# Performance work log

Measured on AMD Instinct MI355X. Metric: run time of the kernel, lower is better.

The kernel has to match this reference:

```python
import jax, jax.numpy as jnp
import numpy as np

EPS = 1e-5

def _conv(x, w, pad):
    # x: [B,C,H,W] NCHW, w: [O,I,kh,kw] OIHW
    return jax.lax.conv_general_dilated(
        x, w, (1, 1), [(pad, pad), (pad, pad)],
        dimension_numbers=('NCHW', 'OIHW', 'NCHW'))

def _bn(x, g, b, m, v):
    # eval-mode batchnorm folded into scale/shift
    s = g * jax.lax.rsqrt(v + EPS)
    return x * s[None, :, None, None] + (b - m * s)[None, :, None, None]

def _cbr(x, w, g, b, m, v):
    # Convolution block from CornerNet: conv3x3(pad=1, no bias) + BN + ReLU
    return jax.nn.relu(_bn(_conv(x, w, 1), g, b, m, v))


def setup_inputs() -> dict:
    key = jax.random.key(0)
    B, Cin, C, H, W = 4, 256, 256, 128, 128
    kdims = {'up': (C, Cin, 3, 3), 'down': (C, Cin, 3, 3),
             'p': (C, C, 3, 3), 'c1': (C, Cin, 1, 1), 'c2': (C, C, 3, 3)}
    inp = {'x': jax.random.normal(key, (B, Cin, H, W), dtype=jnp.float32)}
    for i, n in enumerate(['up', 'down', 'p', 'c1', 'c2']):
        ks = jax.random.split(jax.random.fold_in(key, i + 1), 5)
        inp['w_' + n] = jax.random.normal(ks[0], kdims[n], dtype=jnp.float32) * 0.02
        inp['g_' + n] = 1.0 + 0.1 * jax.random.normal(ks[1], (C,), dtype=jnp.float32)
        inp['b_' + n] = 0.1 * jax.random.normal(ks[2], (C,), dtype=jnp.float32)
        inp['m_' + n] = 0.1 * jax.random.normal(ks[3], (C,), dtype=jnp.float32)
        inp['v_' + n] = 0.5 + jax.random.uniform(ks[4], (C,), dtype=jnp.float32)
    return inp


def reference(x,
              w_up, g_up, b_up, m_up, v_up,
              w_down, g_down, b_down, m_down, v_down,
              w_p, g_p, b_p, m_p, v_p,
              w_c1, g_c1, b_c1, m_c1, v_c1,
              w_c2, g_c2, b_c2, m_c2, v_c2):
    # up branch: conv-bn-relu then LeftPool (reverse cummax over W) then RightPool (cummax over W)
    up = _cbr(x, w_up, g_up, b_up, m_up, v_up)
    up = jax.lax.cummax(up, axis=3, reverse=True)   # LeftPool
    up = jax.lax.cummax(up, axis=3)                 # RightPool
    # down branch: conv-bn-relu then TopPool (reverse cummax over H) then BottomPool (cummax over H)
    down = _cbr(x, w_down, g_down, b_down, m_down, v_down)
    down = jax.lax.cummax(down, axis=2, reverse=True)  # TopPool
    down = jax.lax.cummax(down, axis=2)                # BottomPool
    # merge path: 3x3 conv + BN on pooled sum
    merge = _bn(_conv(up + down, w_p, 1), g_p, b_p, m_p, v_p)
    # shortcut path: 1x1 conv + BN on input
    bn1 = _bn(_conv(x, w_c1, 0), g_c1, b_c1, m_c1, v_c1)
    relu1 = jax.nn.relu(merge + bn1)
    # output Convolution block
    return _cbr(relu1, w_c2, g_c2, b_c2, m_c2, v_c2)
```

## Files before the change

### kernel.cpp

```cpp
#include <hip/hip_runtime.h>

typedef unsigned short u16;
typedef __attribute__((ext_vector_type(8))) short bf16x8;
typedef __attribute__((ext_vector_type(4))) float f32x4;


__device__ __forceinline__ u16 f2bf(float f) {
  unsigned u = __float_as_uint(f);
  unsigned r = u + 0x7fffu + ((u >> 16) & 1u);
  return (u16)(r >> 16);
}

__device__ __forceinline__ void gll16(const char* g, char* l) {
  __builtin_amdgcn_global_load_lds((const __attribute__((address_space(1))) void*)g,
                                   (__attribute__((address_space(3))) void*)l, 16, 0, 0);
}

__global__ void bn_prep_kernel(const float* __restrict__ g, const float* __restrict__ b,
                               const float* __restrict__ m, const float* __restrict__ v,
                               float* __restrict__ st) {
  int c = threadIdx.x;
  float s = g[c] * rsqrtf(v[c] + 1e-5f);
  st[c] = s;
  st[256 + c] = b[c] - m[c] * s;
}

__global__ void bn_fix_kernel(float* __restrict__ st) {
  int c = threadIdx.x;
  st[2 * 512 + 256 + c] += st[3 * 512 + 256 + c];
  st[3 * 512 + c] = st[3 * 512 + c] / st[2 * 512 + c];
}

__global__ void wprep3_kernel(const float* __restrict__ w, u16* __restrict__ dst) {
  int idx = blockIdx.x * 256 + threadIdx.x;
  int blk = idx >> 13, iu = idx & 8191;
  int co = iu >> 5, w32 = iu & 31, slot = w32 >> 3, e = w32 & 7;
  int q = slot ^ ((co >> 1) & 3);
  int kc = blk & 3, t = blk >> 2;
  int dwi = t % 3, t2 = t / 3, d = t2 % 3, half = t2 / 3;
  int s = d * 3 + dwi;
  int ci = half * 128 + kc * 32 + q * 8 + e;
  dst[idx] = f2bf(w[(co * 256 + ci) * 9 + s]);
}

__global__ void wprep1_kernel(const float* __restrict__ w, u16* __restrict__ dst,
                              const float* __restrict__ ratio) {
  int idx = blockIdx.x * 256 + threadIdx.x;
  int blk = idx >> 13, iu = idx & 8191;
  int co = iu >> 5, w32 = iu & 31, slot = w32 >> 3, e = w32 & 7;
  int q = slot ^ ((co >> 1) & 3);
  int kc = blk & 3, half = blk >> 2;
  int ci = half * 128 + kc * 32 + q * 8 + e;
  dst[idx] = f2bf(w[co * 256 + ci] * ratio[co]);
}

__global__ __launch_bounds__(256) void nchw_to_nhwc_kernel(const float* __restrict__ x,
                                                           char* __restrict__ xb) {
  __shared__ __align__(16) u16 tl[128 * 130];
  int bh = blockIdx.x; int b = bh >> 7, h = bh & 127;
  int t = threadIdx.x;
  for (int half = 0; half < 2; ++half) {
    __syncthreads();
    for (int i = 0; i < 64; ++i) {
      int cil = i * 2 + (t >> 7);
      int ci = half * 128 + cil;
      int w = t & 127;
      tl[w * 130 + cil] = f2bf(x[(size_t)((b * 256 + ci) * 128 + h) * 128 + w]);
    }
    __syncthreads();
    char* plane = xb + (size_t)(b * 128 + h) * 65536 + half * 32768;
    for (int i = 0; i < 32; ++i) {
      int w = i * 4 + (t >> 6);
      int c2 = (t & 63) * 2;
      unsigned v = *(const unsigned*)&tl[w * 130 + c2];
      *(unsigned*)(plane + w * 256 + ((c2 * 2) ^ (((w + 1) & 7) << 4))) = v;
    }
  }
}

__device__ __forceinline__ void conv_pipeline(const char* inB1, const char* inB2,
                                              const char* wA1, const char* wA2,
                                              int h, int nsteps, char* lds,
                                              f32x4 (&acc)[4][4]) {
  const int t = threadIdx.x;
  const int wv = t >> 6, lane = t & 63;
  const int lane15 = lane & 15, q = lane >> 4;
  const int coq = wv >> 1, wh = wv & 1;
  char* ldsB = lds;
  char* ldsA0 = lds + 33280;

  int aOff[4];
#pragma unroll
  for (int f = 0; f < 4; ++f) {
    int ra = coq * 64 + f * 16 + lane15;
    aOff[f] = ra * 64 + ((q ^ ((ra >> 1) & 3)) << 4);
  }
  int wpb[4];
#pragma unroll
  for (int f = 0; f < 4; ++f) wpb[f] = wh * 64 + f * 16 + lane15;

  auto stageA = [&](int step, int buf) {
    const char* src = (step < 72) ? (wA1 + (size_t)step * 16384)
                                  : (wA2 + (size_t)(step - 72) * 16384);
    char* dst = ldsA0 + buf * 16384 + wv * 1024;
    const char* g = src + wv * 1024 + lane * 16;
    gll16(g, dst);
    gll16(g + 8192, dst + 8192);
  };
  auto stageB = [&](const char* plane) {
    if (plane) {
      char* dst = ldsB + 256 + wv * 1024;
      const char* g = plane + wv * 1024 + lane * 16;
#pragma unroll
      for (int r = 0; r < 4; ++r) gll16(g + r * 8192, dst + r * 8192);
      int4 z = {0, 0, 0, 0};
      if (t < 16) *(int4*)(ldsB + t * 16) = z;
      else if (t < 32) *(int4*)(ldsB + 33024 + (t - 16) * 16) = z;
    } else {
      int4 z = {0, 0, 0, 0};
#pragma unroll
      for (int r = 0; r < 4; ++r) *(int4*)(ldsB + r * 8192 + t * 16) = z;
      if (t < 32) *(int4*)(ldsB + 32768 + t * 16) = z;
    }
  };

  int cur = 0, i = 0;
  for (int outer = 0; outer < 6; ++outer) {
    const int half = (outer >= 3) ? 1 : 0;
    const int d = outer - half * 3;
    const int hs = h + d - 1;
    const char* plane = (hs >= 0 && hs < 128)
                            ? inB1 + (size_t)hs * 65536 + (size_t)half * 32768
                            : nullptr;
    stageB(plane);
    if (outer == 0) stageA(0, 0);
    __syncthreads();
#pragma unroll
    for (int dwi = 0; dwi < 3; ++dwi) {
#pragma unroll
      for (int kc = 0; kc < 4; ++kc) {
        if (i + 1 < nsteps) stageA(i + 1, cur ^ 1);
        bf16x8 af[4], bf[4];
        const char* lA = ldsA0 + cur * 16384;
#pragma unroll
        for (int f = 0; f < 4; ++f) af[f] = *(const bf16x8*)(lA + aOff[f]);
#pragma unroll
        for (int f = 0; f < 4; ++f) {
          int wp = wpb[f] + dwi;
          bf[f] = *(const bf16x8*)(ldsB + wp * 256 + ((kc * 64 + q * 16) ^ ((wp & 7) << 4)));
        }
#pragma unroll
        for (int fm = 0; fm < 4; ++fm)
#pragma unroll
          for (int fn = 0; fn < 4; ++fn)
            acc[fm][fn] = __builtin_amdgcn_mfma_f32_16x16x32_bf16(af[fm], bf[fn], acc[fm][fn], 0, 0, 0);
        __syncthreads();
        cur ^= 1;
        ++i;
      }
    }
  }
  if (nsteps > 72) {
    for (int half2 = 0; half2 < 2; ++half2) {
      stageB(inB2 + (size_t)h * 65536 + (size_t)half2 * 32768);
      __syncthreads();
#pragma unroll
      for (int kc = 0; kc < 4; ++kc) {
        if (i + 1 < nsteps) stageA(i + 1, cur ^ 1);
        bf16x8 af[4], bf[4];
        const char* lA = ldsA0 + cur * 16384;
#pragma unroll
        for (int f = 0; f < 4; ++f) af[f] = *(const bf16x8*)(lA + aOff[f]);
#pragma unroll
        for (int f = 0; f < 4; ++f) {
          int wp = wpb[f] + 1;
          bf[f] = *(const bf16x8*)(ldsB + wp * 256 + ((kc * 64 + q * 16) ^ ((wp & 7) << 4)));
        }
#pragma unroll
        for (int fm = 0; fm < 4; ++fm)
#pragma unroll
          for (int fn = 0; fn < 4; ++fn)
            acc[fm][fn] = __builtin_amdgcn_mfma_f32_16x16x32_bf16(af[fm], bf[fn], acc[fm][fn], 0, 0, 0);
        __syncthreads();
        cur ^= 1;
        ++i;
      }
    }
  }
}

__device__ __forceinline__ void zero_acc(f32x4 (&acc)[4][4]) {
  f32x4 z = {0.f, 0.f, 0.f, 0.f};
#pragma unroll
  for (int i = 0; i < 4; ++i)
#pragma unroll
    for (int j = 0; j < 4; ++j) acc[i][j] = z;
}

__device__ __forceinline__ void store_pad_relu(f32x4 (&acc)[4][4], const float* __restrict__ st,
                                               int b, int h, char* __restrict__ out) {
  const int t = threadIdx.x, lane = t & 63, wv = t >> 6;
  const int lane15 = lane & 15, q = lane >> 4, coq = wv >> 1, wh = wv & 1;
  char* plane = out + (size_t)(b * 128 + h) * 65536;
#pragma unroll
  for (int fm = 0; fm < 4; ++fm) {
    int co = coq * 64 + fm * 16 + q * 4;
    float ss[4], tt[4];
#pragma unroll
    for (int r = 0; r < 4; ++r) { ss[r] = st[co + r]; tt[r] = st[256 + co + r]; }
#pragma unroll
    for (int fn = 0; fn < 4; ++fn) {
      int w = wh * 64 + fn * 16 + lane15;
      short4 o;
      o.x = (short)f2bf(fmaxf(acc[fm][fn][0] * ss[0] + tt[0], 0.f));
      o.y = (short)f2bf(fmaxf(acc[fm][fn][1] * ss[1] + tt[1], 0.f));
      o.z = (short)f2bf(fmaxf(acc[fm][fn][2] * ss[2] + tt[2], 0.f));
      o.w = (short)f2bf(fmaxf(acc[fm][fn][3] * ss[3] + tt[3], 0.f));
      *(short4*)(plane + (co >> 7) * 32768 + w * 256 + (((co & 127) * 2) ^ (((w + 1) & 7) << 4))) = o;
    }
  }
}

__global__ __launch_bounds__(512, 4) void conv_up_kernel(const char* __restrict__ xb,
                                                         const char* __restrict__ wp,
                                                         const float* __restrict__ st,
                                                         float* __restrict__ rmax) {
  __shared__ __align__(16) char lds[66048];
  int swz = (blockIdx.x & 7) * 64 + (blockIdx.x >> 3);
  int b = swz >> 7, h = swz & 127;
  f32x4 acc[4][4];
  zero_acc(acc);
  conv_pipeline(xb + (size_t)b * 8388608, nullptr, wp, nullptr, h, 72, lds, acc);

  const int t = threadIdx.x, lane = t & 63, wv = t >> 6;
  const int lane15 = lane & 15, q = lane >> 4, coq = wv >> 1, wh = wv & 1;
  float* rlds = (float*)lds;
  __syncthreads();
#pragma unroll
  for (int fm = 0; fm < 4; ++fm) {
    int co = coq * 64 + fm * 16 + q * 4;
#pragma unroll
    for (int r = 0; r < 4; ++r) {
      float ss = st[co + r], tt = st[256 + co + r];
      float v = 0.f;
#pragma unroll
      for (int fn = 0; fn < 4; ++fn) v = fmaxf(v, acc[fm][fn][r] * ss + tt);
      v = fmaxf(v, __shfl_xor(v, 1));
      v = fmaxf(v, __shfl_xor(v, 2));
      v = fmaxf(v, __shfl_xor(v, 4));
      v = fmaxf(v, __shfl_xor(v, 8));
      if (lane15 == 0) rlds[wh * 256 + co + r] = v;
    }
  }
  __syncthreads();
  if (t < 256) rmax[(size_t)(b * 128 + h) * 256 + t] = fmaxf(rlds[t], rlds[256 + t]);
}

__global__ __launch_bounds__(512, 4) void conv_down_kernel(const char* __restrict__ xb,
                                                           const char* __restrict__ wp,
                                                           const float* __restrict__ st,
                                                           char* __restrict__ out) {
  __shared__ __align__(16) char lds[66048];
  int swz = (blockIdx.x & 7) * 64 + (blockIdx.x >> 3);
  int b = swz >> 7, h = swz & 127;
  f32x4 acc[4][4];
  zero_acc(acc);
  conv_pipeline(xb + (size_t)b * 8388608, nullptr, wp, nullptr, h, 72, lds, acc);
  store_pad_relu(acc, st, b, h, out);
}

__global__ __launch_bounds__(256) void colmax_kernel(const char* __restrict__ dp,
                                                     float* __restrict__ cmax) {
  int bw = blockIdx.x; int b = bw >> 7, w = bw & 127;
  int c = threadIdx.x;
  size_t base = (size_t)b * 8388608 + (size_t)(c >> 7) * 32768 + w * 256 +
                (((c & 127) * 2) ^ (((w + 1) & 7) << 4));
  float m = 0.f;
  for (int h = 0; h < 128; ++h) {
    u16 raw = *(const u16*)(dp + base + (size_t)h * 65536);
    m = fmaxf(m, __uint_as_float(((unsigned)raw) << 16));
  }
  cmax[(size_t)(b * 128 + w) * 256 + c] = m;
}

__global__ __launch_bounds__(256) void pooled_kernel(const float* __restrict__ rmax,
                                                     const float* __restrict__ cmax,
                                                     char* __restrict__ dp) {
  int bh = blockIdx.x; int b = bh >> 7, h = bh & 127;
  int c = threadIdx.x;
  float rm = rmax[(size_t)(b * 128 + h) * 256 + c];
  char* plane = dp + (size_t)(b * 128 + h) * 65536 + (c >> 7) * 32768;
  int cb = (c & 127) * 2;
  for (int w = 0; w < 128; ++w) {
    float v = rm + cmax[(size_t)(b * 128 + w) * 256 + c];
    *(u16*)(plane + w * 256 + (cb ^ (((w + 1) & 7) << 4))) = f2bf(v);
  }
}

__global__ __launch_bounds__(512, 4) void conv_merge_kernel(const char* __restrict__ dp,
                                                            const char* __restrict__ xb,
                                                            const char* __restrict__ wp_p,
                                                            const char* __restrict__ wp_c1,
                                                            const float* __restrict__ st,
                                                            char* __restrict__ out) {
  __shared__ __align__(16) char lds[66048];
  int swz = (blockIdx.x & 7) * 64 + (blockIdx.x >> 3);
  int b = swz >> 7, h = swz & 127;
  f32x4 acc[4][4];
  zero_acc(acc);
  conv_pipeline(dp + (size_t)b * 8388608, xb + (size_t)b * 8388608, wp_p, wp_c1, h, 80, lds, acc);
  store_pad_relu(acc, st, b, h, out);
}

__global__ __launch_bounds__(512, 4) void conv_c2_kernel(const char* __restrict__ relu1,
                                                         const char* __restrict__ wp,
                                                         const float* __restrict__ st,
                                                         float* __restrict__ out) {
  __shared__ __align__(16) char lds[66048];
  int swz = (blockIdx.x & 7) * 64 + (blockIdx.x >> 3);
  int b = swz >> 7, h = swz & 127;
  f32x4 acc[4][4];
  zero_acc(acc);
  conv_pipeline(relu1 + (size_t)b * 8388608, nullptr, wp, nullptr, h, 72, lds, acc);

  const int t = threadIdx.x, lane = t & 63, wv = t >> 6;
  const int lane15 = lane & 15, q = lane >> 4, coq = wv >> 1, wh = wv & 1;
  float* tl = (float*)lds;
  for (int g = 0; g < 16; ++g) {
    __syncthreads();
    if (coq == (g >> 2)) {
      int fm = g & 3;
      int co = coq * 64 + fm * 16 + q * 4;
#pragma unroll
      for (int r = 0; r < 4; ++r) {
        float ss = st[co + r], tt = st[256 + co + r];
#pragma unroll
        for (int fn = 0; fn < 4; ++fn) {
          int w = wh * 64 + fn * 16 + lane15;
          tl[(q * 4 + r) * 132 + w] = fmaxf(acc[fm][fn][r] * ss + tt, 0.f);
        }
      }
    }
    __syncthreads();
    int row = t >> 5, wq = (t & 31) * 4;
    float4 vv = *(float4*)&tl[row * 132 + wq];
    *(float4*)(out + (size_t)((b * 256 + g * 16 + row) * 128 + h) * 128 + wq) = vv;
  }
}

extern "C" void kernel_launch(void* const* d_in, const int* in_sizes, int n_in,
                              void* d_out, int out_size, void* d_ws, size_t ws_size,
                              hipStream_t stream) {
  (void)in_sizes; (void)n_in; (void)out_size; (void)ws_size;
  const float* x    = (const float*)d_in[0];
  const float* w_up = (const float*)d_in[1];
  const float* w_dn = (const float*)d_in[6];
  const float* w_p  = (const float*)d_in[11];
  const float* w_c1 = (const float*)d_in[16];
  const float* w_c2 = (const float*)d_in[21];

  char* ws = (char*)d_ws;
  char* xb    = ws;
  char* dp    = ws + 33554432ull;
  char* relu1 = ws + 67108864ull;
  u16* wp_up  = (u16*)(ws + 100663296ull);
  u16* wp_dn  = (u16*)(ws + 101842944ull);
  u16* wp_p   = (u16*)(ws + 103022592ull);
  u16* wp_c2  = (u16*)(ws + 104202240ull);
  u16* wp_c1  = (u16*)(ws + 105381888ull);
  float* st   = (float*)(ws + 105512960ull);
  float* rmax = (float*)(ws + 105523200ull);
  float* cmax = (float*)(ws + 106047488ull);

  bn_prep_kernel<<<1, 256, 0, stream>>>((const float*)d_in[2], (const float*)d_in[3],
                                        (const float*)d_in[4], (const float*)d_in[5], st);
  bn_prep_kernel<<<1, 256, 0, stream>>>((const float*)d_in[7], (const float*)d_in[8],
                                        (const float*)d_in[9], (const float*)d_in[10], st + 512);
  bn_prep_kernel<<<1, 256, 0, stream>>>((const float*)d_in[12], (const float*)d_in[13],
                                        (const float*)d_in[14], (const float*)d_in[15], st + 1024);
  bn_prep_kernel<<<1, 256, 0, stream>>>((const float*)d_in[17], (const float*)d_in[18],
                                        (const float*)d_in[19], (const float*)d_in[20], st + 1536);
  bn_prep_kernel<<<1, 256, 0, stream>>>((const float*)d_in[22], (const float*)d_in[23],
                                        (const float*)d_in[24], (const float*)d_in[25], st + 2048);
  bn_fix_kernel<<<1, 256, 0, stream>>>(st);

  wprep3_kernel<<<2304, 256, 0, stream>>>(w_up, wp_up);
  wprep3_kernel<<<2304, 256, 0, stream>>>(w_dn, wp_dn);
  wprep3_kernel<<<2304, 256, 0, stream>>>(w_p, wp_p);
  wprep3_kernel<<<2304, 256, 0, stream>>>(w_c2, wp_c2);
  wprep1_kernel<<<256, 256, 0, stream>>>(w_c1, wp_c1, st + 1536);

  nchw_to_nhwc_kernel<<<512, 256, 0, stream>>>(x, xb);

  conv_up_kernel<<<512, 512, 0, stream>>>(xb, (const char*)wp_up, st, rmax);
  conv_down_kernel<<<512, 512, 0, stream>>>(xb, (const char*)wp_dn, st + 512, dp);
  colmax_kernel<<<512, 256, 0, stream>>>(dp, cmax);
  pooled_kernel<<<512, 256, 0, stream>>>(rmax, cmax, dp);
  conv_merge_kernel<<<512, 512, 0, stream>>>(dp, xb, (const char*)wp_p, (const char*)wp_c1,
                                             st + 1024, relu1);
  conv_c2_kernel<<<512, 512, 0, stream>>>(relu1, (const char*)wp_c2, st + 2048, (float*)d_out);
}
```

Before: 429.1 us.

## Split conv kernels across output-channel halves with 256-thread blocks

Each conv kernel now runs a 2D grid where blockIdx.y picks one half of the 256 output channels. Blocks shrink to 256 threads and a smaller LDS footprint. The weight prep kernels lay the weights out per half, and the staging code is rewritten for 256 threads. This doubles block count and aims to raise occupancy, at the cost of loading each input row plane twice, once per channel half.

```diff
diff --git a/kernel.cpp b/kernel.cpp
--- a/kernel.cpp
+++ b/kernel.cpp
@@ -33,24 +33,28 @@
 
 __global__ void wprep3_kernel(const float* __restrict__ w, u16* __restrict__ dst) {
   int idx = blockIdx.x * 256 + threadIdx.x;
-  int blk = idx >> 13, iu = idx & 8191;
-  int co = iu >> 5, w32 = iu & 31, slot = w32 >> 3, e = w32 & 7;
-  int q = slot ^ ((co >> 1) & 3);
-  int kc = blk & 3, t = blk >> 2;
-  int dwi = t % 3, t2 = t / 3, d = t2 % 3, half = t2 / 3;
+  int blk = idx >> 12, iu = idx & 4095;
+  int co_l = iu >> 5, w32 = iu & 31, slot = w32 >> 3, e = w32 & 7;
+  int q = slot ^ ((co_l >> 1) & 3);
+  int cohalf = blk / 72, step = blk % 72;
+  int outer = step / 12, rr = step % 12, dwi = rr >> 2, kc = rr & 3;
+  int half = outer / 3, d = outer % 3;
   int s = d * 3 + dwi;
   int ci = half * 128 + kc * 32 + q * 8 + e;
+  int co = cohalf * 128 + co_l;
   dst[idx] = f2bf(w[(co * 256 + ci) * 9 + s]);
 }
 
 __global__ void wprep1_kernel(const float* __restrict__ w, u16* __restrict__ dst,
                               const float* __restrict__ ratio) {
   int idx = blockIdx.x * 256 + threadIdx.x;
-  int blk = idx >> 13, iu = idx & 8191;
-  int co = iu >> 5, w32 = iu & 31, slot = w32 >> 3, e = w32 & 7;
-  int q = slot ^ ((co >> 1) & 3);
-  int kc = blk & 3, half = blk >> 2;
-  int ci = half * 128 + kc * 32 + q * 8 + e;
+  int blk = idx >> 12, iu = idx & 4095;
+  int co_l = iu >> 5, w32 = iu & 31, slot = w32 >> 3, e = w32 & 7;
+  int q = slot ^ ((co_l >> 1) & 3);
+  int cohalf = blk >> 3, j = blk & 7;
+  int half2 = j >> 2, kc = j & 3;
+  int ci = half2 * 128 + kc * 32 + q * 8 + e;
+  int co = cohalf * 128 + co_l;
   dst[idx] = f2bf(w[co * 256 + ci] * ratio[co]);
 }
 
@@ -78,6 +82,29 @@
   }
 }
 
+__device__ __forceinline__ void stage_a(const char* wA1, const char* wA2, int step,
+                                        char* ldsA0, int buf, int t) {
+  const char* src = (step < 72) ? (wA1 + (size_t)step * 8192)
+                                : (wA2 + (size_t)(step - 72) * 8192);
+  char* dst = ldsA0 + buf * 8192 + t * 16;
+  const char* g = src + t * 16;
+  gll16(g, dst);
+  gll16(g + 4096, dst + 4096);
+}
+
+__device__ __forceinline__ void stage_b(const char* plane, char* ldsB, int t) {
+  if (plane) {
+    char* dst = ldsB + 256 + t * 16;
+    const char* g = plane + t * 16;
+#pragma unroll
+    for (int r = 0; r < 8; ++r) gll16(g + r * 4096, dst + r * 4096);
+  } else {
+    int4 z = {0, 0, 0, 0};
+#pragma unroll
+    for (int r = 0; r < 8; ++r) *(int4*)(ldsB + 256 + r * 4096 + t * 16) = z;
+  }
+}
+
 __device__ __forceinline__ void conv_pipeline(const char* inB1, const char* inB2,
                                               const char* wA1, const char* wA2,
                                               int h, int nsteps, char* lds,
@@ -99,30 +126,11 @@
 #pragma unroll
   for (int f = 0; f < 4; ++f) wpb[f] = wh * 64 + f * 16 + lane15;
 
-  auto stageA = [&](int step, int buf) {
-    const char* src = (step < 72) ? (wA1 + (size_t)step * 16384)
-                                  : (wA2 + (size_t)(step - 72) * 16384);
-    char* dst = ldsA0 + buf * 16384 + wv * 1024;
-    const char* g = src + wv * 1024 + lane * 16;
-    gll16(g, dst);
-    gll16(g + 8192, dst + 8192);
-  };
-  auto stageB = [&](const char* plane) {
-    if (plane) {
-      char* dst = ldsB + 256 + wv * 1024;
-      const char* g = plane + wv * 1024 + lane * 16;
-#pragma unroll
-      for (int r = 0; r < 4; ++r) gll16(g + r * 8192, dst + r * 8192);
-      int4 z = {0, 0, 0, 0};
-      if (t < 16) *(int4*)(ldsB + t * 16) = z;
-      else if (t < 32) *(int4*)(ldsB + 33024 + (t - 16) * 16) = z;
-    } else {
-      int4 z = {0, 0, 0, 0};
-#pragma unroll
-      for (int r = 0; r < 4; ++r) *(int4*)(ldsB + r * 8192 + t * 16) = z;
-      if (t < 32) *(int4*)(ldsB + 32768 + t * 16) = z;
-    }
-  };
+  {
+    int4 z = {0, 0, 0, 0};
+    if (t < 16) *(int4*)(ldsB + t * 16) = z;
+    else if (t < 32) *(int4*)(ldsB + 33024 + (t - 16) * 16) = z;
+  }
 
   int cur = 0, i = 0;
   for (int outer = 0; outer < 6; ++outer) {
@@ -132,16 +140,16 @@
     const char* plane = (hs >= 0 && hs < 128)
                             ? inB1 + (size_t)hs * 65536 + (size_t)half * 32768
                             : nullptr;
-    stageB(plane);
-    if (outer == 0) stageA(0, 0);
+    stage_b(plane, ldsB, t);
+    if (outer == 0) stage_a(wA1, wA2, 0, ldsA0, 0, t);
     __syncthreads();
 #pragma unroll
-    for (int dwi = 0; dwi < 3; ++dwi) {
+    for (int dwi = 0; dwi < 3; ++dwi)
 #pragma unroll
       for (int kc = 0; kc < 4; ++kc) {
-        if (i + 1 < nsteps) stageA(i + 1, cur ^ 1);
+        if (i + 1 < nsteps) stage_a(wA1, wA2, i + 1, ldsA0, cur ^ 1, t);
         bf16x8 af[4], bf[4];
-        const char* lA = ldsA0 + cur * 16384;
+        const char* lA = ldsA0 + cur * 8192;
 #pragma unroll
         for (int f = 0; f < 4; ++f) af[f] = *(const bf16x8*)(lA + aOff[f]);
 #pragma unroll
@@ -158,17 +166,16 @@
         cur ^= 1;
         ++i;
       }
-    }
   }
   if (nsteps > 72) {
     for (int half2 = 0; half2 < 2; ++half2) {
-      stageB(inB2 + (size_t)h * 65536 + (size_t)half2 * 32768);
+      stage_b(inB2 + (size_t)h * 65536 + (size_t)half2 * 32768, ldsB, t);
       __syncthreads();
 #pragma unroll
       for (int kc = 0; kc < 4; ++kc) {
-        if (i + 1 < nsteps) stageA(i + 1, cur ^ 1);
+        if (i + 1 < nsteps) stage_a(wA1, wA2, i + 1, ldsA0, cur ^ 1, t);
         bf16x8 af[4], bf[4];
-        const char* lA = ldsA0 + cur * 16384;
+        const char* lA = ldsA0 + cur * 8192;
 #pragma unroll
         for (int f = 0; f < 4; ++f) af[f] = *(const bf16x8*)(lA + aOff[f]);
 #pragma unroll
@@ -198,13 +205,14 @@
 }
 
 __device__ __forceinline__ void store_pad_relu(f32x4 (&acc)[4][4], const float* __restrict__ st,
-                                               int b, int h, char* __restrict__ out) {
+                                               int cohalf, int b, int h, char* __restrict__ out) {
   const int t = threadIdx.x, lane = t & 63, wv = t >> 6;
   const int lane15 = lane & 15, q = lane >> 4, coq = wv >> 1, wh = wv & 1;
-  char* plane = out + (size_t)(b * 128 + h) * 65536;
+  char* plane = out + (size_t)(b * 128 + h) * 65536 + cohalf * 32768;
 #pragma unroll
   for (int fm = 0; fm < 4; ++fm) {
-    int co = coq * 64 + fm * 16 + q * 4;
+    int co_l = coq * 64 + fm * 16 + q * 4;
+    int co = cohalf * 128 + co_l;
     float ss[4], tt[4];
 #pragma unroll
     for (int r = 0; r < 4; ++r) { ss[r] = st[co + r]; tt[r] = st[256 + co + r]; }
@@ -216,21 +224,23 @@
       o.y = (short)f2bf(fmaxf(acc[fm][fn][1] * ss[1] + tt[1], 0.f));
       o.z = (short)f2bf(fmaxf(acc[fm][fn][2] * ss[2] + tt[2], 0.f));
       o.w = (short)f2bf(fmaxf(acc[fm][fn][3] * ss[3] + tt[3], 0.f));
-      *(short4*)(plane + (co >> 7) * 32768 + w * 256 + (((co & 127) * 2) ^ (((w + 1) & 7) << 4))) = o;
-    }
-  }
-}
-
-__global__ __launch_bounds__(512, 4) void conv_up_kernel(const char* __restrict__ xb,
+      *(short4*)(plane + w * 256 + ((co_l * 2) ^ (((w + 1) & 7) << 4))) = o;
+    }
+  }
+}
+
+__global__ __launch_bounds__(256, 3) void conv_up_kernel(const char* __restrict__ xb,
                                                          const char* __restrict__ wp,
                                                          const float* __restrict__ st,
                                                          float* __restrict__ rmax) {
-  __shared__ __align__(16) char lds[66048];
+  __shared__ __align__(16) char lds[49664];
   int swz = (blockIdx.x & 7) * 64 + (blockIdx.x >> 3);
   int b = swz >> 7, h = swz & 127;
+  int cohalf = blockIdx.y;
   f32x4 acc[4][4];
   zero_acc(acc);
-  conv_pipeline(xb + (size_t)b * 8388608, nullptr, wp, nullptr, h, 72, lds, acc);
+  conv_pipeline(xb + (size_t)b * 8388608, nullptr, wp + (size_t)cohalf * 589824, nullptr,
+                h, 72, lds, acc);
 
   const int t = threadIdx.x, lane = t & 63, wv = t >> 6;
   const int lane15 = lane & 15, q = lane >> 4, coq = wv >> 1, wh = wv & 1;
@@ -238,7 +248,8 @@
   __syncthreads();
 #pragma unroll
   for (int fm = 0; fm < 4; ++fm) {
-    int co = coq * 64 + fm * 16 + q * 4;
+    int co_l = coq * 64 + fm * 16 + q * 4;
+    int co = cohalf * 128 + co_l;
 #pragma unroll
     for (int r = 0; r < 4; ++r) {
       float ss = st[co + r], tt = st[256 + co + r];
@@ -249,24 +260,27 @@
       v = fmaxf(v, __shfl_xor(v, 2));
       v = fmaxf(v, __shfl_xor(v, 4));
       v = fmaxf(v, __shfl_xor(v, 8));
-      if (lane15 == 0) rlds[wh * 256 + co + r] = v;
+      if (lane15 == 0) rlds[wh * 128 + co_l + r] = v;
     }
   }
   __syncthreads();
-  if (t < 256) rmax[(size_t)(b * 128 + h) * 256 + t] = fmaxf(rlds[t], rlds[256 + t]);
-}
-
-__global__ __launch_bounds__(512, 4) void conv_down_kernel(const char* __restrict__ xb,
+  if (t < 128)
+    rmax[(size_t)(b * 128 + h) * 256 + cohalf * 128 + t] = fmaxf(rlds[t], rlds[128 + t]);
+}
+
+__global__ __launch_bounds__(256, 3) void conv_down_kernel(const char* __restrict__ xb,
                                                            const char* __restrict__ wp,
                                                            const float* __restrict__ st,
                                                            char* __restrict__ out) {
-  __shared__ __align__(16) char lds[66048];
+  __shared__ __align__(16) char lds[49664];
   int swz = (blockIdx.x & 7) * 64 + (blockIdx.x >> 3);
   int b = swz >> 7, h = swz & 127;
+  int cohalf = blockIdx.y;
   f32x4 acc[4][4];
   zero_acc(acc);
-  conv_pipeline(xb + (size_t)b * 8388608, nullptr, wp, nullptr, h, 72, lds, acc);
-  store_pad_relu(acc, st, b, h, out);
+  conv_pipeline(xb + (size_t)b * 8388608, nullptr, wp + (size_t)cohalf * 589824, nullptr,
+                h, 72, lds, acc);
+  store_pad_relu(acc, st, cohalf, b, h, out);
 }
 
 __global__ __launch_bounds__(256) void colmax_kernel(const char* __restrict__ dp,
@@ -297,40 +311,46 @@
   }
 }
 
-__global__ __launch_bounds__(512, 4) void conv_merge_kernel(const char* __restrict__ dp,
+__global__ __launch_bounds__(256, 3) void conv_merge_kernel(const char* __restrict__ dp,
                                                             const char* __restrict__ xb,
                                                             const char* __restrict__ wp_p,
                                                             const char* __restrict__ wp_c1,
                                                             const float* __restrict__ st,
                                                             char* __restrict__ out) {
-  __shared__ __align__(16) char lds[66048];
+  __shared__ __align__(16) char lds[49664];
   int swz = (blockIdx.x & 7) * 64 + (blockIdx.x >> 3);
   int b = swz >> 7, h = swz & 127;
+  int cohalf = blockIdx.y;
   f32x4 acc[4][4];
   zero_acc(acc);
-  conv_pipeline(dp + (size_t)b * 8388608, xb + (size_t)b * 8388608, wp_p, wp_c1, h, 80, lds, acc);
-  store_pad_relu(acc, st, b, h, out);
-}
-
-__global__ __launch_bounds__(512, 4) void conv_c2_kernel(const char* __restrict__ relu1,
+  conv_pipeline(dp + (size_t)b * 8388608, xb + (size_t)b * 8388608,
+                wp_p + (size_t)cohalf * 589824, wp_c1 + (size_t)cohalf * 65536,
+                h, 80, lds, acc);
+  store_pad_relu(acc, st, cohalf, b, h, out);
+}
+
+__global__ __launch_bounds__(256, 3) void conv_c2_kernel(const char* __restrict__ relu1,
                                                          const char* __restrict__ wp,
                                                          const float* __restrict__ st,
                                                          float* __restrict__ out) {
-  __shared__ __align__(16) char lds[66048];
+  __shared__ __align__(16) char lds[49664];
   int swz = (blockIdx.x & 7) * 64 + (blockIdx.x >> 3);
   int b = swz >> 7, h = swz & 127;
+  int cohalf = blockIdx.y;
   f32x4 acc[4][4];
   zero_acc(acc);
-  conv_pipeline(relu1 + (size_t)b * 8388608, nullptr, wp, nullptr, h, 72, lds, acc);
+  conv_pipeline(relu1 + (size_t)b * 8388608, nullptr, wp + (size_t)cohalf * 589824, nullptr,
+                h, 72, lds, acc);
 
   const int t = threadIdx.x, lane = t & 63, wv = t >> 6;
   const int lane15 = lane & 15, q = lane >> 4, coq = wv >> 1, wh = wv & 1;
   float* tl = (float*)lds;
-  for (int g = 0; g < 16; ++g) {
+  for (int g = 0; g < 8; ++g) {
     __syncthreads();
     if (coq == (g >> 2)) {
       int fm = g & 3;
-      int co = coq * 64 + fm * 16 + q * 4;
+      int co_l = coq * 64 + fm * 16 + q * 4;
+      int co = cohalf * 128 + co_l;
 #pragma unroll
       for (int r = 0; r < 4; ++r) {
         float ss = st[co + r], tt = st[256 + co + r];
@@ -342,9 +362,13 @@
       }
     }
     __syncthreads();
-    int row = t >> 5, wq = (t & 31) * 4;
-    float4 vv = *(float4*)&tl[row * 132 + wq];
-    *(float4*)(out + (size_t)((b * 256 + g * 16 + row) * 128 + h) * 128 + wq) = vv;
+    int row = t >> 4, ch = t & 15;
+    int co = cohalf * 128 + g * 16 + row;
+    float* dst = out + (size_t)((b * 256 + co) * 128 + h) * 128 + ch * 8;
+    float4 p0 = *(float4*)&tl[row * 132 + ch * 8];
+    float4 p1 = *(float4*)&tl[row * 132 + ch * 8 + 4];
+    *(float4*)dst = p0;
+    *(float4*)(dst + 4) = p1;
   }
 }
 
@@ -392,11 +416,12 @@
 
   nchw_to_nhwc_kernel<<<512, 256, 0, stream>>>(x, xb);
 
-  conv_up_kernel<<<512, 512, 0, stream>>>(xb, (const char*)wp_up, st, rmax);
-  conv_down_kernel<<<512, 512, 0, stream>>>(xb, (const char*)wp_dn, st + 512, dp);
+  conv_up_kernel<<<dim3(512, 2), 256, 0, stream>>>(xb, (const char*)wp_up, st, rmax);
+  conv_down_kernel<<<dim3(512, 2), 256, 0, stream>>>(xb, (const char*)wp_dn, st + 512, dp);
   colmax_kernel<<<512, 256, 0, stream>>>(dp, cmax);
   pooled_kernel<<<512, 256, 0, stream>>>(rmax, cmax, dp);
-  conv_merge_kernel<<<512, 512, 0, stream>>>(dp, xb, (const char*)wp_p, (const char*)wp_c1,
-                                             st + 1024, relu1);
-  conv_c2_kernel<<<512, 512, 0, stream>>>(relu1, (const char*)wp_c2, st + 2048, (float*)d_out);
-}
+  conv_merge_kernel<<<dim3(512, 2), 256, 0, stream>>>(dp, xb, (const char*)wp_p,
+                                                      (const char*)wp_c1, st + 1024, relu1);
+  conv_c2_kernel<<<dim3(512, 2), 256, 0, stream>>>(relu1, (const char*)wp_c2, st + 2048,
+                                                   (float*)d_out);
+}
```

Measured after the change: 397.6 us. 1.08x faster.
